# Performance work log

Hardware: AMD Instinct MI355X
Metric: run time of the kernel (lower is better)

The kernel has to match this reference:

```python
import jax, jax.numpy as jnp
import numpy as np


def setup_inputs() -> dict:
    key = jax.random.key(0)
    k1, k2, k3, k4 = jax.random.split(key, 4)
    pi = np.float32(np.pi)
    return {
        "bii": pi * jax.random.uniform(k1, (1,), dtype=jnp.float32),
        "bjj": pi * jax.random.uniform(k2, (1,), dtype=jnp.float32),
        "bij_real": pi * jax.random.uniform(k3, (1,), dtype=jnp.float32),
        "bij_img": pi * jax.random.uniform(k4, (1,), dtype=jnp.float32),
        "conn_i": 123,
        "conn_j": 4567,
        "N": 8192,
    }


def _block_exp(bii, bjj, bij_real, bij_img):
    """Closed-form exp(1j*H) for Hermitian 2x2 H = [[a, c],[conj(c), b]].

    exp(1j*H) = e^{1j*t} * (cos(r) I + 1j * sin(r)/r * (H - t I)),
    t = (a+b)/2, r = sqrt(((a-b)/2)^2 + |c|^2). Exact since B is zero
    outside the 2x2 block, matching torch.matrix_exp(1j*B).
    """
    a = bii[0]
    b = bjj[0]
    cr = bij_real[0]
    ci = bij_img[0]
    t = 0.5 * (a + b)
    d = 0.5 * (a - b)
    r = jnp.sqrt(d * d + cr * cr + ci * ci)
    safe_r = jnp.where(r > 0, r, jnp.ones_like(r))
    sinc = jnp.where(r > 0, jnp.sin(r) / safe_r, jnp.ones_like(r))
    cosr = jnp.cos(r)
    phase = jnp.exp(1j * t.astype(jnp.complex64))  # complex64 scalar
    c = (cr + 1j * ci).astype(jnp.complex64)
    e_ii = phase * (cosr + 1j * sinc * d)
    e_jj = phase * (cosr - 1j * sinc * d)
    e_ij = phase * (1j * sinc) * c
    e_ji = phase * (1j * sinc) * jnp.conj(c)
    return e_ii, e_jj, e_ij, e_ji


def reference(bii, bjj, bij_real, bij_img, conn_i, conn_j, N):
    e_ii, e_jj, e_ij, e_ji = _block_exp(bii, bjj, bij_real, bij_img)
    V = jnp.eye(N, dtype=jnp.complex64)
    rows = jnp.array([conn_i, conn_j, conn_i, conn_j])
    cols = jnp.array([conn_i, conn_j, conn_j, conn_i])
    vals = jnp.stack([e_ii, e_jj, e_ij, e_ji]).astype(jnp.complex64)
    V = V.at[rows, cols].set(vals)
    return V
```

## Files before the change

### kernel.cpp

```cpp
#include <hip/hip_runtime.h>
#include <math.h>

typedef float vfloat4 __attribute__((ext_vector_type(4)));

__device__ __forceinline__ void set_lane(vfloat4& v, int k, float val) {
    switch (k) {
        case 0: v.x = val; break;
        case 1: v.y = val; break;
        case 2: v.z = val; break;
        case 3: v.w = val; break;
    }
}

__global__ __launch_bounds__(256) void fill_all_kernel(
    vfloat4* __restrict__ out4, int out_size,
    const float* __restrict__ bii,
    const float* __restrict__ bjj,
    const float* __restrict__ bij_real,
    const float* __restrict__ bij_img,
    const int* __restrict__ conn_i,
    const int* __restrict__ conn_j,
    const int* __restrict__ Np)
{
    const int n = Np[0];
    const int stride = out_size / n;
    const int mult = stride / n;
    const int ls = 31 - __clz(stride);
    const int mask = stride - 1;
    const int i = conn_i[0];
    const int j = conn_j[0];

    const int n_f4 = out_size >> 2;
    const int tid = blockIdx.x * 256 + threadIdx.x;
    const int nth = gridDim.x * 256;

    #pragma unroll 4
    for (int q = tid; q < n_f4; q += nth) {
        const int f = q << 2;
        const int row = f >> ls;
        const int o = f & mask;

        vfloat4 v = {0.f, 0.f, 0.f, 0.f};

        const int k = row * mult - o;
        if ((unsigned)k < 4u) set_lane(v, k, 1.0f);

        if (row == i || row == j) {
            const float a  = bii[0];
            const float b  = bjj[0];
            const float cr = bij_real[0];
            const float ci = bij_img[0];

            const float t  = 0.5f * (a + b);
            const float dd = 0.5f * (a - b);
            const float r  = sqrtf(dd * dd + cr * cr + ci * ci);
            const float sinc = (r > 0.f) ? (sinf(r) / r) : 1.0f;
            const float cosr = cosf(r);
            const float pr = cosf(t);
            const float pim = sinf(t);

            const float sd = sinc * dd;
            float eii_r = pr * cosr - pim * sd;
            float eii_i = pr * sd + pim * cosr;
            float ejj_r = pr * cosr + pim * sd;
            float ejj_i = -pr * sd + pim * cosr;
            const float scr = -sinc * ci;
            const float sci =  sinc * cr;
            float eij_r = pr * scr - pim * sci;
            float eij_i = pr * sci + pim * scr;
            const float sjr =  sinc * ci;
            const float sji =  sinc * cr;
            const float eji_r = pr * sjr - pim * sji;
            const float eji_i = pr * sji + pim * sjr;

            if (i == j) {
                eii_r = eji_r; eii_i = eji_i;
                ejj_r = eji_r; ejj_i = eji_i;
                eij_r = eji_r; eij_i = eji_i;
            }

            float c0r, c0i, c1r, c1i;
            if (row == i) { c0r = eii_r; c0i = eii_i; c1r = eij_r; c1i = eij_i; }
            else          { c0r = eji_r; c0i = eji_i; c1r = ejj_r; c1i = ejj_i; }

            if (mult == 2) {
                const int k0 = 2 * i - o;
                if ((unsigned)k0 < 4u) { set_lane(v, k0, c0r); set_lane(v, k0 + 1, c0i); }
                const int k1 = 2 * j - o;
                if ((unsigned)k1 < 4u) { set_lane(v, k1, c1r); set_lane(v, k1 + 1, c1i); }
            } else {
                const int k0 = i - o;
                if ((unsigned)k0 < 4u) set_lane(v, k0, c0r);
                const int k1 = j - o;
                if ((unsigned)k1 < 4u) set_lane(v, k1, c1r);
            }
        }

        __builtin_nontemporal_store(v, out4 + q);
    }
}

extern "C" void kernel_launch(void* const* d_in, const int* in_sizes, int n_in,
                              void* d_out, int out_size, void* d_ws, size_t ws_size,
                              hipStream_t stream) {
    const float* bii      = (const float*)d_in[0];
    const float* bjj      = (const float*)d_in[1];
    const float* bij_real = (const float*)d_in[2];
    const float* bij_img  = (const float*)d_in[3];
    const int*   conn_i   = (const int*)d_in[4];
    const int*   conn_j   = (const int*)d_in[5];
    const int*   Np       = (const int*)d_in[6];

    const int n_f4 = out_size >> 2;
    int blocks = (n_f4 + 255) / 256;
    if (blocks > 2048) blocks = 2048;

    fill_all_kernel<<<dim3(blocks), dim3(256), 0, stream>>>(
        (vfloat4*)d_out, out_size, bii, bjj, bij_real, bij_img,
        conn_i, conn_j, Np);
}
```

Before: 288.0 us.

## Assign one block per row and precompute per-row nonzero vectors

Result: faster. 267.1 us (-7.2%).

```diff
diff --git a/kernel.cpp b/kernel.cpp
--- a/kernel.cpp
+++ b/kernel.cpp
@@ -12,8 +12,8 @@
     }
 }
 
-__global__ __launch_bounds__(256) void fill_all_kernel(
-    vfloat4* __restrict__ out4, int out_size,
+__global__ __launch_bounds__(256) void fill_rows_kernel(
+    float* __restrict__ out, int out_size,
     const float* __restrict__ bii,
     const float* __restrict__ bjj,
     const float* __restrict__ bij_real,
@@ -25,27 +25,24 @@
     const int n = Np[0];
     const int stride = out_size / n;
     const int mult = stride / n;
-    const int ls = 31 - __clz(stride);
-    const int mask = stride - 1;
     const int i = conn_i[0];
     const int j = conn_j[0];
 
-    const int n_f4 = out_size >> 2;
-    const int tid = blockIdx.x * 256 + threadIdx.x;
-    const int nth = gridDim.x * 256;
+    const int row = blockIdx.x;
+    if (row >= n) return;
+    const bool isI = (row == i);
+    const bool isJ = (row == j);
 
-    #pragma unroll 4
-    for (int q = tid; q < n_f4; q += nth) {
-        const int f = q << 2;
-        const int row = f >> ls;
-        const int o = f & mask;
+    int s0, s1 = -1;
+    vfloat4 w0 = {0.f, 0.f, 0.f, 0.f};
+    vfloat4 w1 = {0.f, 0.f, 0.f, 0.f};
+    {
+        int c0, c1 = -1;
+        float v0r, v0i = 0.f, v1r = 0.f, v1i = 0.f;
 
-        vfloat4 v = {0.f, 0.f, 0.f, 0.f};
-
-        const int k = row * mult - o;
-        if ((unsigned)k < 4u) set_lane(v, k, 1.0f);
-
-        if (row == i || row == j) {
+        if (!isI && !isJ) {
+            c0 = mult * row; v0r = 1.0f;
+        } else {
             const float a  = bii[0];
             const float b  = bjj[0];
             const float cr = bij_real[0];
@@ -56,47 +53,63 @@
             const float r  = sqrtf(dd * dd + cr * cr + ci * ci);
             const float sinc = (r > 0.f) ? (sinf(r) / r) : 1.0f;
             const float cosr = cosf(r);
-            const float pr = cosf(t);
+            const float pr  = cosf(t);
             const float pim = sinf(t);
 
             const float sd = sinc * dd;
-            float eii_r = pr * cosr - pim * sd;
-            float eii_i = pr * sd + pim * cosr;
-            float ejj_r = pr * cosr + pim * sd;
-            float ejj_i = -pr * sd + pim * cosr;
+            const float eii_r = pr * cosr - pim * sd;
+            const float eii_i = pr * sd + pim * cosr;
+            const float ejj_r = pr * cosr + pim * sd;
+            const float ejj_i = -pr * sd + pim * cosr;
             const float scr = -sinc * ci;
             const float sci =  sinc * cr;
-            float eij_r = pr * scr - pim * sci;
-            float eij_i = pr * sci + pim * scr;
+            const float eij_r = pr * scr - pim * sci;
+            const float eij_i = pr * sci + pim * scr;
             const float sjr =  sinc * ci;
             const float sji =  sinc * cr;
             const float eji_r = pr * sjr - pim * sji;
             const float eji_i = pr * sji + pim * sjr;
 
             if (i == j) {
-                eii_r = eji_r; eii_i = eji_i;
-                ejj_r = eji_r; ejj_i = eji_i;
-                eij_r = eji_r; eij_i = eji_i;
-            }
-
-            float c0r, c0i, c1r, c1i;
-            if (row == i) { c0r = eii_r; c0i = eii_i; c1r = eij_r; c1i = eij_i; }
-            else          { c0r = eji_r; c0i = eji_i; c1r = ejj_r; c1i = ejj_i; }
-
-            if (mult == 2) {
-                const int k0 = 2 * i - o;
-                if ((unsigned)k0 < 4u) { set_lane(v, k0, c0r); set_lane(v, k0 + 1, c0i); }
-                const int k1 = 2 * j - o;
-                if ((unsigned)k1 < 4u) { set_lane(v, k1, c1r); set_lane(v, k1 + 1, c1i); }
+                c0 = mult * i; v0r = eji_r; v0i = eji_i;
+            } else if (isI) {
+                c0 = mult * i; v0r = eii_r; v0i = eii_i;
+                c1 = mult * j; v1r = eij_r; v1i = eij_i;
             } else {
-                const int k0 = i - o;
-                if ((unsigned)k0 < 4u) set_lane(v, k0, c0r);
-                const int k1 = j - o;
-                if ((unsigned)k1 < 4u) set_lane(v, k1, c1r);
+                c0 = mult * i; v0r = eji_r; v0i = eji_i;
+                c1 = mult * j; v1r = ejj_r; v1i = ejj_i;
             }
         }
 
-        __builtin_nontemporal_store(v, out4 + q);
+        s0 = c0 >> 2;
+        const int p0 = c0 & 3;
+        set_lane(w0, p0, v0r);
+        if (mult == 2) set_lane(w0, p0 + 1, v0i);
+
+        if (c1 >= 0) {
+            const int sB = c1 >> 2;
+            const int p1 = c1 & 3;
+            if (sB == s0) {
+                set_lane(w0, p1, v1r);
+                if (mult == 2) set_lane(w0, p1 + 1, v1i);
+            } else {
+                s1 = sB;
+                set_lane(w1, p1, v1r);
+                if (mult == 2) set_lane(w1, p1 + 1, v1i);
+            }
+        }
+    }
+
+    vfloat4* __restrict__ rowp = (vfloat4*)(out + (size_t)row * stride);
+    const int nf4 = stride >> 2;
+    const vfloat4 zero = {0.f, 0.f, 0.f, 0.f};
+
+    #pragma unroll 4
+    for (int q = threadIdx.x; q < nf4; q += 256) {
+        vfloat4 v = zero;
+        if (q == s0) v = w0;
+        if (q == s1) v = w1;
+        rowp[q] = v;
     }
 }
 
@@ -111,11 +124,7 @@
     const int*   conn_j   = (const int*)d_in[5];
     const int*   Np       = (const int*)d_in[6];
 
-    const int n_f4 = out_size >> 2;
-    int blocks = (n_f4 + 255) / 256;
-    if (blocks > 2048) blocks = 2048;
-
-    fill_all_kernel<<<dim3(blocks), dim3(256), 0, stream>>>(
-        (vfloat4*)d_out, out_size, bii, bjj, bij_real, bij_img,
+    fill_rows_kernel<<<dim3(8192), dim3(256), 0, stream>>>(
+        (float*)d_out, out_size, bii, bjj, bij_real, bij_img,
         conn_i, conn_j, Np);
 }
```
